# Optimization experiments

Measured on AMD Instinct MI355X. Metric: run time of the kernel, lower is better.

## Reference

```python
import jax, jax.numpy as jnp
import numpy as np

TOP_K = 8


def setup_inputs() -> dict:
    key = jax.random.key(0)
    k1, k2 = jax.random.split(key)
    hidden_states = jax.random.normal(k1, (4, 4096, 4096), dtype=jnp.float32)
    weight = jax.random.normal(k2, (64, 4096), dtype=jnp.float32) * 0.02
    return {"hidden_states": hidden_states, "weight": weight}


def reference(hidden_states, weight):
    # Flatten [B, S, H] -> [T, H]; gating math is done in float32 (matches .float()).
    h = hidden_states.shape[-1]
    x = hidden_states.reshape(-1, h).astype(jnp.float32)
    # Router logits: [T, E] = [T, H] @ [H, E]
    logits = jnp.einsum('th,eh->te', x, weight.astype(jnp.float32))
    scores = jax.nn.softmax(logits, axis=-1)
    # Top-k expert selection (greedy router)
    topk_weight, topk_idx = jax.lax.top_k(scores, TOP_K)  # [T, K], [T, K]
    # Normalize top-k probabilities (norm_topk_prob=True)
    denom = jnp.sum(topk_weight, axis=-1, keepdims=True) + 1e-20
    topk_weight = topk_weight / denom
    return topk_weight, topk_idx
```

## Files before the change

kernel.cpp:

```cpp
#include <hip/hip_runtime.h>
#include <math.h>

typedef float  f32x4  __attribute__((ext_vector_type(4)));
typedef int    i32x4  __attribute__((ext_vector_type(4)));

#define H      4096
#define E      64
#define TOPK   8
#define TILE_T 32
#define CK     256
#define MS     4
#define NCH    16

__global__ __launch_bounds__(256)
void prep_w(const float* __restrict__ Wg, signed char* __restrict__ Wb)
{
  int n = blockIdx.x * 256 + threadIdx.x;
  int kgrp = n & 3, m = (n >> 2) & 63, e = n >> 8;
  const float* wp = Wg + e * 4096 + m * 64 + kgrp * 16;
  signed char lb[5][16];
  #pragma unroll
  for (int s = 0; s < 16; ++s) {
    long long v = (long long)rint((double)wp[s] * 2199023255552.0);
    #pragma unroll
    for (int j = 0; j < 4; ++j) {
      signed char b = (signed char)(v & 0xff);
      lb[j][s] = b;
      v = (v - b) >> 8;
    }
    lb[4][s] = (signed char)v;
  }
  int lanei = (kgrp << 4) | (e & 15);
  int eq = e >> 4;
  #pragma unroll
  for (int j = 0; j < 5; ++j) {
    i32x4 d;
    #pragma unroll
    for (int r = 0; r < 4; ++r)
      d[r] = (lb[j][4*r] & 0xFF) | ((lb[j][4*r+1] & 0xFF) << 8)
           | ((lb[j][4*r+2] & 0xFF) << 16) | ((lb[j][4*r+3] & 0xFF) << 24);
    *(i32x4*)(Wb + (((size_t)(m * 4 + eq) * 5 + j) << 10) + lanei * 16) = d;
  }
}

__global__ __launch_bounds__(64)
void comp_w(const float* __restrict__ Wg, double* __restrict__ compT)
{
  int e = blockIdx.x;
  int lane = threadIdx.x;
  double s = 0.0;
  #pragma unroll 4
  for (int i = 0; i < 64; ++i)
    s += rint((double)Wg[e * 4096 + i * 64 + lane] * 2199023255552.0);
  #pragma unroll
  for (int off = 32; off >= 1; off >>= 1)
    s += __shfl_xor(s, off);
  if (lane == 0) compT[e] = 8421504.0 * s;
}

__global__ __launch_bounds__(512)
void moe_gate_i8(const float* __restrict__ X, const signed char* __restrict__ Wb,
                 const double* __restrict__ compT, float* __restrict__ out,
                 int n_tokens)
{
  __shared__ char sm[65536];
  double* Ls = (double*)sm;

  const int tid  = threadIdx.x;
  const int lane = tid & 63;
  const int w    = tid >> 6;
  const int t0   = blockIdx.x * TILE_T;
  const int l15  = lane & 15;
  const int kg   = lane >> 4;

  i32x4 z = {0, 0, 0, 0};
  int lab = l15 * 0x01010101;
  i32x4 onev = {0x01010101, 0x01010101, 0x01010101, 0x01010101};
  i32x4 labv = {lab, lab, lab, lab};
  i32x4 pr = __builtin_amdgcn_mfma_i32_16x16x64_i8(labv, onev, z, 0, 0, 0);
  i32x4 pc = __builtin_amdgcn_mfma_i32_16x16x64_i8(onev, labv, z, 0, 0, 0);
  int qrow[4], qcol[4];
  #pragma unroll
  for (int r = 0; r < 4; ++r) { qrow[r] = pr[r] >> 6; qcol[r] = pc[r] >> 6; }

  i32x4 aA3 = z, aA4 = z, aA5 = z, aA6 = z, aA7 = z;
  i32x4 aB3 = z, aB4 = z, aB5 = z, aB6 = z, aB7 = z;
  const signed char* bpp = Wb + (w & 3) * 5120 + lane * 16;

  const int tt = (w - 4) * 8 + (lane >> 3);
  const int ks = lane & 7;
  const float* xp = X + (size_t)(t0 + (tt & 31)) * H + ks * 32;
  const int swzw = ks << 4;
  char* wb0 = sm + ((ks * 2 + 0) << 11) + (((tt & 31) << 4) ^ swzw);
  char* wb1 = sm + ((ks * 2 + 1) << 11) + (((tt & 31) << 4) ^ swzw);

  #define CONV(xr, hf, W0, W1, W2, W3)                                        \
  {                                                                           \
    unsigned w32[16];                                                         \
    _Pragma("unroll")                                                         \
    for (int r = 0; r < 4; ++r) {                                             \
      f32x4 xv = xr[(hf) * 4 + r];                                            \
      _Pragma("unroll")                                                       \
      for (int jj = 0; jj < 4; ++jj)                                          \
        w32[r*4+jj] = ((unsigned)(int)(xv[jj] * 268435456.0f)) ^ 0x00808080u; \
    }                                                                         \
    _Pragma("unroll")                                                         \
    for (int r = 0; r < 4; ++r) {                                             \
      unsigned u0 = w32[4*r], u1 = w32[4*r+1], u2 = w32[4*r+2], u3 = w32[4*r+3];\
      unsigned p01, p23;                                                      \
      p01 = __builtin_amdgcn_perm(u1, u0, 0x04000400u);                       \
      p23 = __builtin_amdgcn_perm(u3, u2, 0x04000400u);                       \
      W0[r] = (int)__builtin_amdgcn_perm(p23, p01, 0x05040100u);              \
      p01 = __builtin_amdgcn_perm(u1, u0, 0x05010501u);                       \
      p23 = __builtin_amdgcn_perm(u3, u2, 0x05010501u);                       \
      W1[r] = (int)__builtin_amdgcn_perm(p23, p01, 0x05040100u);              \
      p01 = __builtin_amdgcn_perm(u1, u0, 0x06020602u);                       \
      p23 = __builtin_amdgcn_perm(u3, u2, 0x06020602u);                       \
      W2[r] = (int)__builtin_amdgcn_perm(p23, p01, 0x05040100u);              \
      p01 = __builtin_amdgcn_perm(u1, u0, 0x07030703u);                       \
      p23 = __builtin_amdgcn_perm(u3, u2, 0x07030703u);                       \
      W3[r] = (int)__builtin_amdgcn_perm(p23, p01, 0x05040100u);              \
    }                                                                         \
  }

  #define PRODUCE(c_, wbuf_)                                                  \
  {                                                                           \
    f32x4 xr[8];                                                              \
    _Pragma("unroll")                                                         \
    for (int q = 0; q < 8; ++q)                                               \
      xr[q] = *(const f32x4*)(xp + (size_t)(c_) * CK + 4 * q);                \
    i32x4 U0, U1, U2, U3, V0, V1, V2, V3;                                     \
    CONV(xr, 0, U0, U1, U2, U3);                                              \
    CONV(xr, 1, V0, V1, V2, V3);                                              \
    char* b0_ = wb0 + ((wbuf_) << 15);                                        \
    char* b1_ = wb1 + ((wbuf_) << 15);                                        \
    *(i32x4*)(b0_ + 0x000) = U0;                                              \
    *(i32x4*)(b0_ + 0x200) = U1;                                              \
    *(i32x4*)(b0_ + 0x400) = U2;                                              \
    *(i32x4*)(b0_ + 0x600) = U3;                                              \
    *(i32x4*)(b1_ + 0x000) = V0;                                              \
    *(i32x4*)(b1_ + 0x200) = V1;                                              \
    *(i32x4*)(b1_ + 0x400) = V2;                                              \
    *(i32x4*)(b1_ + 0x600) = V3;                                              \
  }

  if (w >= 4) PRODUCE(0, 0);
  __syncthreads();

  for (int c = 0; c < NCH; ++c) {
    const int cur = c & 1;
    if (w < 4) {
      const char* base = sm + (cur << 15);
      #pragma unroll
      for (int m = 0; m < MS; ++m) {
        const int kq   = 4 * m + kg;
        const int swzr = ((kq >> 1) & 7) << 4;
        const char* abase = base + (kq << 11) + (((l15 << 4) ^ swzr));
        i32x4 b0 = *(const i32x4*)(bpp);
        i32x4 b1 = *(const i32x4*)(bpp + 1024);
        i32x4 b2 = *(const i32x4*)(bpp + 2048);
        i32x4 b3 = *(const i32x4*)(bpp + 3072);
        i32x4 b4 = *(const i32x4*)(bpp + 4096);
        bpp += 20480;
        i32x4 xA0 = *(const i32x4*)(abase + 0x000);
        i32x4 xA1 = *(const i32x4*)(abase + 0x200);
        i32x4 xA2 = *(const i32x4*)(abase + 0x400);
        i32x4 xA3 = *(const i32x4*)(abase + 0x600);
        i32x4 xB0 = *(const i32x4*)(abase + 0x100);
        i32x4 xB1 = *(const i32x4*)(abase + 0x300);
        i32x4 xB2 = *(const i32x4*)(abase + 0x500);
        i32x4 xB3 = *(const i32x4*)(abase + 0x700);
        aA3 = __builtin_amdgcn_mfma_i32_16x16x64_i8(xA0, b3, aA3, 0, 0, 0);
        aB3 = __builtin_amdgcn_mfma_i32_16x16x64_i8(xB0, b3, aB3, 0, 0, 0);
        aA4 = __builtin_amdgcn_mfma_i32_16x16x64_i8(xA0, b4, aA4, 0, 0, 0);
        aB4 = __builtin_amdgcn_mfma_i32_16x16x64_i8(xB0, b4, aB4, 0, 0, 0);
        aA5 = __builtin_amdgcn_mfma_i32_16x16x64_i8(xA1, b4, aA5, 0, 0, 0);
        aB5 = __builtin_amdgcn_mfma_i32_16x16x64_i8(xB1, b4, aB5, 0, 0, 0);
        aA6 = __builtin_amdgcn_mfma_i32_16x16x64_i8(xA2, b4, aA6, 0, 0, 0);
        aB6 = __builtin_amdgcn_mfma_i32_16x16x64_i8(xB2, b4, aB6, 0, 0, 0);
        aA7 = __builtin_amdgcn_mfma_i32_16x16x64_i8(xA3, b4, aA7, 0, 0, 0);
        aB7 = __builtin_amdgcn_mfma_i32_16x16x64_i8(xB3, b4, aB7, 0, 0, 0);
        aA3 = __builtin_amdgcn_mfma_i32_16x16x64_i8(xA1, b2, aA3, 0, 0, 0);
        aB3 = __builtin_amdgcn_mfma_i32_16x16x64_i8(xB1, b2, aB3, 0, 0, 0);
        aA4 = __builtin_amdgcn_mfma_i32_16x16x64_i8(xA1, b3, aA4, 0, 0, 0);
        aB4 = __builtin_amdgcn_mfma_i32_16x16x64_i8(xB1, b3, aB4, 0, 0, 0);
        aA5 = __builtin_amdgcn_mfma_i32_16x16x64_i8(xA2, b3, aA5, 0, 0, 0);
        aB5 = __builtin_amdgcn_mfma_i32_16x16x64_i8(xB2, b3, aB5, 0, 0, 0);
        aA6 = __builtin_amdgcn_mfma_i32_16x16x64_i8(xA3, b3, aA6, 0, 0, 0);
        aB6 = __builtin_amdgcn_mfma_i32_16x16x64_i8(xB3, b3, aB6, 0, 0, 0);
        aA3 = __builtin_amdgcn_mfma_i32_16x16x64_i8(xA2, b1, aA3, 0, 0, 0);
        aB3 = __builtin_amdgcn_mfma_i32_16x16x64_i8(xB2, b1, aB3, 0, 0, 0);
        aA4 = __builtin_amdgcn_mfma_i32_16x16x64_i8(xA2, b2, aA4, 0, 0, 0);
        aB4 = __builtin_amdgcn_mfma_i32_16x16x64_i8(xB2, b2, aB4, 0, 0, 0);
        aA5 = __builtin_amdgcn_mfma_i32_16x16x64_i8(xA3, b2, aA5, 0, 0, 0);
        aB5 = __builtin_amdgcn_mfma_i32_16x16x64_i8(xB3, b2, aB5, 0, 0, 0);
        aA3 = __builtin_amdgcn_mfma_i32_16x16x64_i8(xA3, b0, aA3, 0, 0, 0);
        aB3 = __builtin_amdgcn_mfma_i32_16x16x64_i8(xB3, b0, aB3, 0, 0, 0);
        aA4 = __builtin_amdgcn_mfma_i32_16x16x64_i8(xA3, b1, aA4, 0, 0, 0);
        aB4 = __builtin_amdgcn_mfma_i32_16x16x64_i8(xB3, b1, aB4, 0, 0, 0);
      }
    } else {
      if (c < NCH - 1) PRODUCE(c + 1, cur ^ 1);
    }
    __syncthreads();
  }
  #undef PRODUCE
  #undef CONV

  if (w < 4) {
    #pragma unroll
    for (int r = 0; r < 4; ++r) {
      int ex = (w & 3) * 16 + qcol[r];
      double pA = (16777216.0          * (double)aA3[r]
                 + 4294967296.0        * (double)aA4[r]
                 + 1099511627776.0     * (double)aA5[r]
                 + 281474976710656.0   * (double)aA6[r]
                 + 72057594037927936.0 * (double)aA7[r]
                 + compT[ex]) * 1.6940658945086007e-21;
      double pB = (16777216.0          * (double)aB3[r]
                 + 4294967296.0        * (double)aB4[r]
                 + 1099511627776.0     * (double)aB5[r]
                 + 281474976710656.0   * (double)aB6[r]
                 + 72057594037927936.0 * (double)aB7[r]
                 + compT[ex]) * 1.6940658945086007e-21;
      Ls[qrow[r] * E + ex]        = pA;
      Ls[(16 + qrow[r]) * E + ex] = pB;
    }
  }
  __syncthreads();

  for (int tt2 = 0; tt2 < 4; tt2++) {
    int t = w * 4 + tt2;
    double val = Ls[t * E + lane];

    double mx = val;
    #pragma unroll
    for (int off = 32; off >= 1; off >>= 1)
      mx = fmax(mx, __shfl_xor(mx, off));

    float p = expf((float)(val - mx));
    float S = p;
    #pragma unroll
    for (int off = 32; off >= 1; off >>= 1)
      S += __shfl_xor(S, off);

    double cur = val;
    float myw = 0.f; int myidx = 0;
    float psum = 0.f;
    #pragma unroll
    for (int r = 0; r < TOPK; r++) {
      double v = cur; int ii = lane;
      #pragma unroll
      for (int off = 32; off >= 1; off >>= 1) {
        double ov = __shfl_xor(v, off);
        int    oi = __shfl_xor(ii, off);
        if (ov > v || (ov == v && oi < ii)) { v = ov; ii = oi; }
      }
      float pw = __shfl(p, ii);
      psum += pw;
      if (lane == r) { myw = pw; myidx = ii; }
      if (lane == ii) cur = -INFINITY;
    }
    float denom = psum + 1e-20f * S;
    if (lane < TOPK) {
      size_t gt = (size_t)(t0 + t);
      out[gt * TOPK + lane] = myw / denom;
      out[(size_t)n_tokens * TOPK + gt * TOPK + lane] = (float)myidx;
    }
  }
}

extern "C" void kernel_launch(void* const* d_in, const int* in_sizes, int n_in,
                              void* d_out, int out_size, void* d_ws, size_t ws_size,
                              hipStream_t stream)
{
  const float* X  = (const float*)d_in[0];
  const float* Wg = (const float*)d_in[1];
  float* out = (float*)d_out;
  signed char* Wb = (signed char*)d_ws;
  double* compT   = (double*)((char*)d_ws + 1310720);
  int n_tokens = in_sizes[0] / H;

  prep_w<<<64, 256, 0, stream>>>(Wg, Wb);
  comp_w<<<64, 64, 0, stream>>>(Wg, compT);
  moe_gate_i8<<<n_tokens / TILE_T, 512, 0, stream>>>(X, Wb, compT, out, n_tokens);
}
```

Before: 136.4 us.

## Prefetch activation chunks two ahead in registers and use lighter LDS-only barriers

The producer warps now issue global loads for chunk c+2 into a second register set before converting and storing chunk c+1 into shared memory. The main loop is unrolled by two so the register sets alternate. __syncthreads is replaced by an lgkmcnt wait plus s_barrier with scheduling fences, so the barrier no longer waits on outstanding global loads. The aim is to hide global-memory latency of the streaming activation reads. The cost is higher register pressure in the producer warps.

Result: slower. 213.9 us (+56.9%).

```diff
diff --git a/kernel.cpp b/kernel.cpp
--- a/kernel.cpp
+++ b/kernel.cpp
@@ -87,12 +87,21 @@
   i32x4 aB3 = z, aB4 = z, aB5 = z, aB6 = z, aB7 = z;
   const signed char* bpp = Wb + (w & 3) * 5120 + lane * 16;
 
-  const int tt = (w - 4) * 8 + (lane >> 3);
+  const int tt = (w & 3) * 8 + (lane >> 3);
   const int ks = lane & 7;
-  const float* xp = X + (size_t)(t0 + (tt & 31)) * H + ks * 32;
+  const float* xp = X + (size_t)(t0 + tt) * H + ks * 32;
   const int swzw = ks << 4;
   char* wb0 = sm + ((ks * 2 + 0) << 11) + (((tt & 31) << 4) ^ swzw);
   char* wb1 = sm + ((ks * 2 + 1) << 11) + (((tt & 31) << 4) ^ swzw);
+
+  f32x4 xrE[8], xrO[8];
+
+  #define ISSUE(c_, xr_)                                                      \
+  {                                                                           \
+    _Pragma("unroll")                                                         \
+    for (int q = 0; q < 8; ++q)                                               \
+      xr_[q] = *(const f32x4*)(xp + (size_t)(c_) * CK + 4 * q);               \
+  }
 
   #define CONV(xr, hf, W0, W1, W2, W3)                                        \
   {                                                                           \
@@ -123,17 +132,13 @@
     }                                                                         \
   }
 
-  #define PRODUCE(c_, wbuf_)                                                  \
-  {                                                                           \
-    f32x4 xr[8];                                                              \
-    _Pragma("unroll")                                                         \
-    for (int q = 0; q < 8; ++q)                                               \
-      xr[q] = *(const f32x4*)(xp + (size_t)(c_) * CK + 4 * q);                \
+  #define PRODUCE_FROM(xr_, bufoff_)                                          \
+  {                                                                           \
     i32x4 U0, U1, U2, U3, V0, V1, V2, V3;                                     \
-    CONV(xr, 0, U0, U1, U2, U3);                                              \
-    CONV(xr, 1, V0, V1, V2, V3);                                              \
-    char* b0_ = wb0 + ((wbuf_) << 15);                                        \
-    char* b1_ = wb1 + ((wbuf_) << 15);                                        \
+    CONV(xr_, 0, U0, U1, U2, U3);                                             \
+    CONV(xr_, 1, V0, V1, V2, V3);                                             \
+    char* b0_ = wb0 + (bufoff_);                                              \
+    char* b1_ = wb1 + (bufoff_);                                              \
     *(i32x4*)(b0_ + 0x000) = U0;                                              \
     *(i32x4*)(b0_ + 0x200) = U1;                                              \
     *(i32x4*)(b0_ + 0x400) = U2;                                              \
@@ -144,68 +149,98 @@
     *(i32x4*)(b1_ + 0x600) = V3;                                              \
   }
 
-  if (w >= 4) PRODUCE(0, 0);
+  #define CONSUME(baseoff_)                                                   \
+  {                                                                           \
+    const char* base_ = sm + (baseoff_);                                      \
+    _Pragma("unroll")                                                         \
+    for (int m = 0; m < MS; ++m) {                                            \
+      const int kq   = 4 * m + kg;                                            \
+      const int swzr = ((kq >> 1) & 7) << 4;                                  \
+      const char* abase = base_ + (kq << 11) + (((l15 << 4) ^ swzr));         \
+      i32x4 b0 = *(const i32x4*)(bpp);                                        \
+      i32x4 b1 = *(const i32x4*)(bpp + 1024);                                 \
+      i32x4 b2 = *(const i32x4*)(bpp + 2048);                                 \
+      i32x4 b3 = *(const i32x4*)(bpp + 3072);                                 \
+      i32x4 b4 = *(const i32x4*)(bpp + 4096);                                 \
+      bpp += 20480;                                                           \
+      i32x4 xA0 = *(const i32x4*)(abase + 0x000);                             \
+      i32x4 xA1 = *(const i32x4*)(abase + 0x200);                             \
+      i32x4 xA2 = *(const i32x4*)(abase + 0x400);                             \
+      i32x4 xA3 = *(const i32x4*)(abase + 0x600);                             \
+      i32x4 xB0 = *(const i32x4*)(abase + 0x100);                             \
+      i32x4 xB1 = *(const i32x4*)(abase + 0x300);                             \
+      i32x4 xB2 = *(const i32x4*)(abase + 0x500);                             \
+      i32x4 xB3 = *(const i32x4*)(abase + 0x700);                             \
+      aA3 = __builtin_amdgcn_mfma_i32_16x16x64_i8(xA0, b3, aA3, 0, 0, 0);     \
+      aB3 = __builtin_amdgcn_mfma_i32_16x16x64_i8(xB0, b3, aB3, 0, 0, 0);     \
+      aA4 = __builtin_amdgcn_mfma_i32_16x16x64_i8(xA0, b4, aA4, 0, 0, 0);     \
+      aB4 = __builtin_amdgcn_mfma_i32_16x16x64_i8(xB0, b4, aB4, 0, 0, 0);     \
+      aA5 = __builtin_amdgcn_mfma_i32_16x16x64_i8(xA1, b4, aA5, 0, 0, 0);     \
+      aB5 = __builtin_amdgcn_mfma_i32_16x16x64_i8(xB1, b4, aB5, 0, 0, 0);     \
+      aA6 = __builtin_amdgcn_mfma_i32_16x16x64_i8(xA2, b4, aA6, 0, 0, 0);     \
+      aB6 = __builtin_amdgcn_mfma_i32_16x16x64_i8(xB2, b4, aB6, 0, 0, 0);     \
+      aA7 = __builtin_amdgcn_mfma_i32_16x16x64_i8(xA3, b4, aA7, 0, 0, 0);     \
+      aB7 = __builtin_amdgcn_mfma_i32_16x16x64_i8(xB3, b4, aB7, 0, 0, 0);     \
+      aA3 = __builtin_amdgcn_mfma_i32_16x16x64_i8(xA1, b2, aA3, 0, 0, 0);     \
+      aB3 = __builtin_amdgcn_mfma_i32_16x16x64_i8(xB1, b2, aB3, 0, 0, 0);     \
+      aA4 = __builtin_amdgcn_mfma_i32_16x16x64_i8(xA1, b3, aA4, 0, 0, 0);     \
+      aB4 = __builtin_amdgcn_mfma_i32_16x16x64_i8(xB1, b3, aB4, 0, 0, 0);     \
+      aA5 = __builtin_amdgcn_mfma_i32_16x16x64_i8(xA2, b3, aA5, 0, 0, 0);     \
+      aB5 = __builtin_amdgcn_mfma_i32_16x16x64_i8(xB2, b3, aB5, 0, 0, 0);     \
+      aA6 = __builtin_amdgcn_mfma_i32_16x16x64_i8(xA3, b3, aA6, 0, 0, 0);     \
+      aB6 = __builtin_amdgcn_mfma_i32_16x16x64_i8(xB3, b3, aB6, 0, 0, 0);     \
+      aA3 = __builtin_amdgcn_mfma_i32_16x16x64_i8(xA2, b1, aA3, 0, 0, 0);     \
+      aB3 = __builtin_amdgcn_mfma_i32_16x16x64_i8(xB2, b1, aB3, 0, 0, 0);     \
+      aA4 = __builtin_amdgcn_mfma_i32_16x16x64_i8(xA2, b2, aA4, 0, 0, 0);     \
+      aB4 = __builtin_amdgcn_mfma_i32_16x16x64_i8(xB2, b2, aB4, 0, 0, 0);     \
+      aA5 = __builtin_amdgcn_mfma_i32_16x16x64_i8(xA3, b2, aA5, 0, 0, 0);     \
+      aB5 = __builtin_amdgcn_mfma_i32_16x16x64_i8(xB3, b2, aB5, 0, 0, 0);     \
+      aA3 = __builtin_amdgcn_mfma_i32_16x16x64_i8(xA3, b0, aA3, 0, 0, 0);     \
+      aB3 = __builtin_amdgcn_mfma_i32_16x16x64_i8(xB3, b0, aB3, 0, 0, 0);     \
+      aA4 = __builtin_amdgcn_mfma_i32_16x16x64_i8(xA3, b1, aA4, 0, 0, 0);     \
+      aB4 = __builtin_amdgcn_mfma_i32_16x16x64_i8(xB3, b1, aB4, 0, 0, 0);     \
+    }                                                                         \
+  }
+
+  #define PHASE_BARRIER                                                       \
+  {                                                                           \
+    asm volatile("s_waitcnt lgkmcnt(0)" ::: "memory");                        \
+    __builtin_amdgcn_sched_barrier(0);                                        \
+    __builtin_amdgcn_s_barrier();                                             \
+    __builtin_amdgcn_sched_barrier(0);                                        \
+  }
+
+  if (w >= 4) {
+    ISSUE(0, xrE);
+    ISSUE(1, xrO);
+    PRODUCE_FROM(xrE, 0);
+  }
   __syncthreads();
 
-  for (int c = 0; c < NCH; ++c) {
-    const int cur = c & 1;
+  for (int c2 = 0; c2 < NCH / 2; ++c2) {
     if (w < 4) {
-      const char* base = sm + (cur << 15);
-      #pragma unroll
-      for (int m = 0; m < MS; ++m) {
-        const int kq   = 4 * m + kg;
-        const int swzr = ((kq >> 1) & 7) << 4;
-        const char* abase = base + (kq << 11) + (((l15 << 4) ^ swzr));
-        i32x4 b0 = *(const i32x4*)(bpp);
-        i32x4 b1 = *(const i32x4*)(bpp + 1024);
-        i32x4 b2 = *(const i32x4*)(bpp + 2048);
-        i32x4 b3 = *(const i32x4*)(bpp + 3072);
-        i32x4 b4 = *(const i32x4*)(bpp + 4096);
-        bpp += 20480;
-        i32x4 xA0 = *(const i32x4*)(abase + 0x000);
-        i32x4 xA1 = *(const i32x4*)(abase + 0x200);
-        i32x4 xA2 = *(const i32x4*)(abase + 0x400);
-        i32x4 xA3 = *(const i32x4*)(abase + 0x600);
-        i32x4 xB0 = *(const i32x4*)(abase + 0x100);
-        i32x4 xB1 = *(const i32x4*)(abase + 0x300);
-        i32x4 xB2 = *(const i32x4*)(abase + 0x500);
-        i32x4 xB3 = *(const i32x4*)(abase + 0x700);
-        aA3 = __builtin_amdgcn_mfma_i32_16x16x64_i8(xA0, b3, aA3, 0, 0, 0);
-        aB3 = __builtin_amdgcn_mfma_i32_16x16x64_i8(xB0, b3, aB3, 0, 0, 0);
-        aA4 = __builtin_amdgcn_mfma_i32_16x16x64_i8(xA0, b4, aA4, 0, 0, 0);
-        aB4 = __builtin_amdgcn_mfma_i32_16x16x64_i8(xB0, b4, aB4, 0, 0, 0);
-        aA5 = __builtin_amdgcn_mfma_i32_16x16x64_i8(xA1, b4, aA5, 0, 0, 0);
-        aB5 = __builtin_amdgcn_mfma_i32_16x16x64_i8(xB1, b4, aB5, 0, 0, 0);
-        aA6 = __builtin_amdgcn_mfma_i32_16x16x64_i8(xA2, b4, aA6, 0, 0, 0);
-        aB6 = __builtin_amdgcn_mfma_i32_16x16x64_i8(xB2, b4, aB6, 0, 0, 0);
-        aA7 = __builtin_amdgcn_mfma_i32_16x16x64_i8(xA3, b4, aA7, 0, 0, 0);
-        aB7 = __builtin_amdgcn_mfma_i32_16x16x64_i8(xB3, b4, aB7, 0, 0, 0);
-        aA3 = __builtin_amdgcn_mfma_i32_16x16x64_i8(xA1, b2, aA3, 0, 0, 0);
-        aB3 = __builtin_amdgcn_mfma_i32_16x16x64_i8(xB1, b2, aB3, 0, 0, 0);
-        aA4 = __builtin_amdgcn_mfma_i32_16x16x64_i8(xA1, b3, aA4, 0, 0, 0);
-        aB4 = __builtin_amdgcn_mfma_i32_16x16x64_i8(xB1, b3, aB4, 0, 0, 0);
-        aA5 = __builtin_amdgcn_mfma_i32_16x16x64_i8(xA2, b3, aA5, 0, 0, 0);
-        aB5 = __builtin_amdgcn_mfma_i32_16x16x64_i8(xB2, b3, aB5, 0, 0, 0);
-        aA6 = __builtin_amdgcn_mfma_i32_16x16x64_i8(xA3, b3, aA6, 0, 0, 0);
-        aB6 = __builtin_amdgcn_mfma_i32_16x16x64_i8(xB3, b3, aB6, 0, 0, 0);
-        aA3 = __builtin_amdgcn_mfma_i32_16x16x64_i8(xA2, b1, aA3, 0, 0, 0);
-        aB3 = __builtin_amdgcn_mfma_i32_16x16x64_i8(xB2, b1, aB3, 0, 0, 0);
-        aA4 = __builtin_amdgcn_mfma_i32_16x16x64_i8(xA2, b2, aA4, 0, 0, 0);
-        aB4 = __builtin_amdgcn_mfma_i32_16x16x64_i8(xB2, b2, aB4, 0, 0, 0);
-        aA5 = __builtin_amdgcn_mfma_i32_16x16x64_i8(xA3, b2, aA5, 0, 0, 0);
-        aB5 = __builtin_amdgcn_mfma_i32_16x16x64_i8(xB3, b2, aB5, 0, 0, 0);
-        aA3 = __builtin_amdgcn_mfma_i32_16x16x64_i8(xA3, b0, aA3, 0, 0, 0);
-        aB3 = __builtin_amdgcn_mfma_i32_16x16x64_i8(xB3, b0, aB3, 0, 0, 0);
-        aA4 = __builtin_amdgcn_mfma_i32_16x16x64_i8(xA3, b1, aA4, 0, 0, 0);
-        aB4 = __builtin_amdgcn_mfma_i32_16x16x64_i8(xB3, b1, aB4, 0, 0, 0);
-      }
+      CONSUME(0);
     } else {
-      if (c < NCH - 1) PRODUCE(c + 1, cur ^ 1);
-    }
-    __syncthreads();
-  }
-  #undef PRODUCE
+      const int c = 2 * c2;
+      if (c < NCH - 2) ISSUE(c + 2, xrE);
+      PRODUCE_FROM(xrO, 32768);
+    }
+    PHASE_BARRIER;
+
+    if (w < 4) {
+      CONSUME(32768);
+    } else {
+      const int c = 2 * c2 + 1;
+      if (c < NCH - 2) ISSUE(c + 2, xrO);
+      if (c < NCH - 1) PRODUCE_FROM(xrE, 0);
+    }
+    PHASE_BARRIER;
+  }
+  #undef ISSUE
   #undef CONV
+  #undef PRODUCE_FROM
+  #undef CONSUME
+  #undef PHASE_BARRIER
 
   if (w < 4) {
     #pragma unroll
```
